# Kernel optimization log

Hardware: AMD Instinct MI355X
Metric: run time of the kernel (lower is better)

## Reference

```python
import math
import jax, jax.numpy as jnp
import numpy as np

CELL = 16
BLOCK = 2
NBINS = 9


def setup_inputs() -> dict:
    key = jax.random.key(0)
    im = jax.random.normal(key, (16, 3, 512, 512), dtype=jnp.float32)
    return {"im": im}


def _l2hys(x):
    # L2 normalize over (bh, bw, bins), clamp at 0.2, renormalize (L2-Hys)
    n1 = jnp.sqrt(jnp.sum(x * x, axis=(-1, -2, -3), keepdims=True))
    t = jnp.minimum(x / (n1 + 1e-10), 0.2)
    n2 = jnp.sqrt(jnp.sum(t * t, axis=(-1, -2, -3), keepdims=True))
    return t / (n2 + 1e-10)


def _hog_forward(im):
    B, C, H, W = im.shape
    cs, nb, bs = CELL, NBINS, BLOCK
    gain = nb / math.pi
    # complex Sobel kernel: real part = x-gradient, imag part = y-gradient
    kx = jnp.array([[-1., 0., 1.], [-2., 0., 2.], [-1., 0., 1.]], jnp.float32)
    ky = jnp.array([[-1., -2., -1.], [0., 0., 0.], [1., 2., 1.]], jnp.float32)
    imp = jnp.pad(im, ((0, 0), (0, 0), (1, 1), (1, 1)), mode="reflect")
    x = imp.reshape(B * C, 1, H + 2, W + 2)
    k = jnp.stack([kx, ky])[:, None]  # (2,1,3,3)
    g = jax.lax.conv_general_dilated(x, k, (1, 1), "VALID")  # (B*C,2,H,W) cross-correlation, matches F.conv2d
    gx = g[:, 0].reshape(B, C, H, W)
    gy = g[:, 1].reshape(B, C, H, W)
    Hc, Wc = H // cs, W // cs
    P = cs * cs

    def unfold_cells(a):  # (B,C,H,W) -> (B,C,Hc,Wc,cs*cs)
        return a.reshape(B, C, Hc, cs, Wc, cs).transpose(0, 1, 2, 4, 3, 5).reshape(B, C, Hc, Wc, P)

    gx = unfold_cells(gx)
    gy = unfold_cells(gy)
    norm = jnp.sqrt(gx * gx + gy * gy)  # complex magnitude
    # channelWise=False: pick the channel with max magnitude per pixel
    idx = jnp.argmax(norm, axis=1, keepdims=True)
    norm = jnp.take_along_axis(norm, idx, axis=1)
    gx = jnp.take_along_axis(gx, idx, axis=1)
    gy = jnp.take_along_axis(gy, idx, axis=1)
    phase = jnp.mod(jnp.arctan2(gy, gx), math.pi)  # complex angle mod pi

    # bilinear soft binning via scatter_add
    edges = jnp.linspace(0.0, math.pi, nb + 1)
    left = jnp.floor(gain * phase).astype(jnp.int32)
    prct = gain * (phase - edges[left])
    li = left % nb
    ri = (left + 1) % nb
    N = B * 1 * Hc * Wc
    rows = jnp.broadcast_to(jnp.arange(N)[:, None], (N, P))
    hist = jnp.zeros((N, nb), norm.dtype)
    hist = hist.at[rows, li.reshape(N, P)].add(((1.0 - prct) * norm).reshape(N, P))
    hist = hist.at[rows, ri.reshape(N, P)].add((prct * norm).reshape(N, P))
    hist = hist.reshape(B, 1, Hc, Wc, nb) / float(P)

    # block normalize: unfold cells into overlapping blocks (stride = blockSize//2)
    step = bs // 2
    Hb = (Hc - bs) // step + 1
    Wb = (Wc - bs) // step + 1
    blocks = jnp.stack(
        [
            jnp.stack(
                [hist[:, :, i:i + step * (Hb - 1) + 1:step, j:j + step * (Wb - 1) + 1:step, :] for j in range(bs)],
                axis=-2,
            )
            for i in range(bs)
        ],
        axis=-3,
    )  # (B,1,Hb,Wb,bs,bs,nb)
    return _l2hys(blocks)


def reference(im):
    return _hog_forward(im)
```

## Files before the change

kernel.cpp:

```cpp
#include <hip/hip_runtime.h>
#include <hip/hip_bf16.h>
#include <math.h>


#define IMG_H 512
#define IMG_W 512
#define NCH 3
#define NB_ 16
#define HC 32
#define WC 32
#define HB 31
#define WB 31
#define NBINS 9

__device__ __forceinline__ int refl(int i, int n) {
    if (i < 0) i = -i;
    else if (i >= n) i = 2 * n - 2 - i;
    return i;
}

__global__ __launch_bounds__(256) void hog_hist_kernel(const float* __restrict__ im,
                                                       float* __restrict__ hist) {
    const int bid = blockIdx.x;
    const int b   = bid >> 8;
    const int cy  = (bid >> 3) & 31;
    const int cxg = bid & 7;

    __shared__ __align__(16) float sT[NCH][18][72];
    __shared__ float swp[4][4][NBINS];

    const int t = threadIdx.x;

    const int y0 = cy * 16 - 1;
    const int x0 = cxg * 64;
    const float* imb = im + (size_t)b * NCH * IMG_H * IMG_W;

    {
        const int x4 = t & 15;
        const int r0 = t >> 4;
#pragma unroll
        for (int k = 0; k < 4; ++k) {
            int rowid = r0 + 16 * k;
            if (rowid < NCH * 18) {
                int c  = rowid / 18;
                int yy = rowid - c * 18;
                int gy = refl(y0 + yy, IMG_H);
                const float4 v = *(const float4*)(imb + ((size_t)c * IMG_H + gy) * IMG_W + x0 + 4 * x4);
                *(float4*)&sT[c][yy][4 + 4 * x4] = v;
            }
        }
        if (t < 108) {
            int side = t & 1;
            int rid  = t >> 1;
            int c    = rid / 18;
            int yy   = rid - c * 18;
            int gy   = refl(y0 + yy, IMG_H);
            int gx   = refl(side ? x0 + 64 : x0 - 1, IMG_W);
            sT[c][yy][side ? 68 : 3] = imb[((size_t)c * IMG_H + gy) * IMG_W + gx];
        }
    }
    __syncthreads();

    const int px = t & 63;
    const int pr = (t >> 6) * 4;
    const int lx = 4 + px;

    float bn[4]  = {-1.0f, -1.0f, -1.0f, -1.0f};
    float bgx[4] = {0, 0, 0, 0};
    float bgy[4] = {0, 0, 0, 0};

#pragma unroll
    for (int c = 0; c < NCH; ++c) {
        float a[6][3];
#pragma unroll
        for (int j = 0; j < 6; ++j) {
            a[j][0] = sT[c][pr + j][lx - 1];
            a[j][1] = sT[c][pr + j][lx];
            a[j][2] = sT[c][pr + j][lx + 1];
        }
#pragma unroll
        for (int p = 0; p < 4; ++p) {
            float gx = (a[p][2] - a[p][0]) + 2.0f * (a[p + 1][2] - a[p + 1][0]) + (a[p + 2][2] - a[p + 2][0]);
            float gy = (a[p + 2][0] - a[p][0]) + 2.0f * (a[p + 2][1] - a[p][1]) + (a[p + 2][2] - a[p][2]);
            float n = sqrtf(gx * gx + gy * gy);
            if (n > bn[p]) { bn[p] = n; bgx[p] = gx; bgy[p] = gy; }
        }
    }

    const float PI_F  = (float)M_PI;
    const float HPI_F = (float)(M_PI / 2.0);
    const float GAIN  = (float)(9.0 / M_PI);
    const float BINW  = (float)(M_PI / 9.0);
    const float C1  = 0.99997726f, C3 = -0.33262347f, C5 = 0.19354346f;
    const float C7  = -0.11643287f, C9 = 0.05265332f, C11 = -0.01172120f;

    float acc[NBINS];
#pragma unroll
    for (int k = 0; k < NBINS; ++k) acc[k] = 0.0f;

#pragma unroll
    for (int p = 0; p < 4; ++p) {
        float gx = bgx[p], gy = bgy[p], n = bn[p];
        float ax = fabsf(gx), ay = fabsf(gy);
        float mn = fminf(ax, ay), mx = fmaxf(ax, ay);
        float r  = __fdividef(mn, mx + 1e-37f);
        float r2 = r * r;
        float at = r * (C1 + r2 * (C3 + r2 * (C5 + r2 * (C7 + r2 * (C9 + r2 * C11)))));
        if (ay > ax) at = HPI_F - at;
        if ((__float_as_uint(gx) ^ __float_as_uint(gy)) & 0x80000000u) at = PI_F - at;

        float fp_ = GAIN * at;
        int left  = (int)floorf(fp_);
        float prct = GAIN * (at - (float)left * BINW);
        int li = (left >= NBINS) ? left - NBINS : left;
        int ri = (li == NBINS - 1) ? 0 : li + 1;

        float w_l = (1.0f - prct) * n;
        float w_r = prct * n;
#pragma unroll
        for (int k = 0; k < NBINS; ++k) {
            acc[k] += (li == k) ? w_l : 0.0f;
            acc[k] += (ri == k) ? w_r : 0.0f;
        }
    }

#pragma unroll
    for (int m = 1; m <= 8; m <<= 1) {
#pragma unroll
        for (int k = 0; k < NBINS; ++k)
            acc[k] += __shfl_xor(acc[k], m, 64);
    }

    const int lane = t & 63;
    const int wv   = t >> 6;
    if ((lane & 15) == 0) {
        const int cl = lane >> 4;
#pragma unroll
        for (int k = 0; k < NBINS; ++k) swp[wv][cl][k] = acc[k];
    }
    __syncthreads();

    if (t < 4 * NBINS) {
        int c_local = t / NBINS;
        int bin     = t - c_local * NBINS;
        float sum = swp[0][c_local][bin] + swp[1][c_local][bin]
                  + swp[2][c_local][bin] + swp[3][c_local][bin];
        int cellX   = cxg * 4 + c_local;
        size_t cell = ((size_t)b * HC + cy) * WC + cellX;
        hist[cell * NBINS + bin] = sum * (1.0f / 256.0f);
    }
}

__global__ __launch_bounds__(256) void hog_norm_kernel(const float* __restrict__ hist,
                                                       float* __restrict__ out) {
    int idx = blockIdx.x * 256 + threadIdx.x;
    if (idx >= NB_ * HB * WB) return;
    int b = idx / (HB * WB);
    int r = idx - b * (HB * WB);
    int i = r / WB;
    int j = r - i * WB;

    float v[36];
    float ss = 0.0f;
#pragma unroll
    for (int bi = 0; bi < 2; ++bi) {
#pragma unroll
        for (int bj = 0; bj < 2; ++bj) {
            const float* hp = hist + (size_t)(((b * HC) + (i + bi)) * WC + (j + bj)) * NBINS;
#pragma unroll
            for (int k = 0; k < NBINS; ++k) {
                float x = hp[k];
                v[(bi * 2 + bj) * NBINS + k] = x;
                ss += x * x;
            }
        }
    }
    float inv1 = 1.0f / (sqrtf(ss) + 1e-10f);
    float ss2 = 0.0f;
#pragma unroll
    for (int k = 0; k < 36; ++k) {
        float tt = fminf(v[k] * inv1, 0.2f);
        v[k] = tt;
        ss2 += tt * tt;
    }
    float inv2 = 1.0f / (sqrtf(ss2) + 1e-10f);
    float* op = out + (size_t)idx * 36;
#pragma unroll
    for (int k = 0; k < 36; ++k) op[k] = v[k] * inv2;
}

extern "C" void kernel_launch(void* const* d_in, const int* in_sizes, int n_in,
                              void* d_out, int out_size, void* d_ws, size_t ws_size,
                              hipStream_t stream) {
    const float* im = (const float*)d_in[0];
    float* out = (float*)d_out;
    float* hist = (float*)d_ws;

    hog_hist_kernel<<<NB_ * HC * 8, 256, 0, stream>>>(im, hist);

    int nout_blocks = NB_ * HB * WB;
    hog_norm_kernel<<<(nout_blocks + 255) / 256, 256, 0, stream>>>(hist, out);
}
```

Baseline: 36.89 us.

## Process two horizontal pixels per thread and use tent-function bin weights

Each block now covers a 128-pixel-wide strip (8 cells), and each thread computes two adjacent pixels, reusing the shared column differences across both Sobel stencils. The soft-binning switches from computing floor/left/right indices to a branchless tent weight fmax(1-|fp-k|,0) per bin, with bin 0 wrapping via fp-9. The shuffle reduction drops one level. This cuts redundant LDS reads and halo loads, but halves the grid size, which lowers parallelism.

```diff
diff --git a/kernel.cpp b/kernel.cpp
--- a/kernel.cpp
+++ b/kernel.cpp
@@ -22,25 +22,24 @@
 __global__ __launch_bounds__(256) void hog_hist_kernel(const float* __restrict__ im,
                                                        float* __restrict__ hist) {
     const int bid = blockIdx.x;
-    const int b   = bid >> 8;
-    const int cy  = (bid >> 3) & 31;
-    const int cxg = bid & 7;
-
-    __shared__ __align__(16) float sT[NCH][18][72];
-    __shared__ float swp[4][4][NBINS];
+    const int b   = bid >> 7;
+    const int cy  = (bid >> 2) & 31;
+    const int cxg = bid & 3;
+
+    __shared__ __align__(16) float sT[NCH][18][136];
+    __shared__ float swp[4][8][NBINS];
 
     const int t = threadIdx.x;
-
     const int y0 = cy * 16 - 1;
-    const int x0 = cxg * 64;
+    const int x0 = cxg * 128;
     const float* imb = im + (size_t)b * NCH * IMG_H * IMG_W;
 
     {
-        const int x4 = t & 15;
-        const int r0 = t >> 4;
-#pragma unroll
-        for (int k = 0; k < 4; ++k) {
-            int rowid = r0 + 16 * k;
+        const int x4 = t & 31;
+        const int rb = t >> 5;
+#pragma unroll
+        for (int k = 0; k < 7; ++k) {
+            int rowid = rb + 8 * k;
             if (rowid < NCH * 18) {
                 int c  = rowid / 18;
                 int yy = rowid - c * 18;
@@ -55,42 +54,59 @@
             int c    = rid / 18;
             int yy   = rid - c * 18;
             int gy   = refl(y0 + yy, IMG_H);
-            int gx   = refl(side ? x0 + 64 : x0 - 1, IMG_W);
-            sT[c][yy][side ? 68 : 3] = imb[((size_t)c * IMG_H + gy) * IMG_W + gx];
+            int gx   = refl(side ? x0 + 128 : x0 - 1, IMG_W);
+            sT[c][yy][side ? 132 : 3] = imb[((size_t)c * IMG_H + gy) * IMG_W + gx];
         }
     }
     __syncthreads();
 
-    const int px = t & 63;
-    const int pr = (t >> 6) * 4;
-    const int lx = 4 + px;
-
-    float bn[4]  = {-1.0f, -1.0f, -1.0f, -1.0f};
-    float bgx[4] = {0, 0, 0, 0};
-    float bgy[4] = {0, 0, 0, 0};
+    const int cp = t & 63;
+    const int rq = t >> 6;
+    const int pr = rq * 4;
+    const int lxm1 = 3 + 2 * cp;
+
+    float bn[2][4], bgx[2][4], bgy[2][4];
+#pragma unroll
+    for (int e = 0; e < 2; ++e)
+#pragma unroll
+        for (int p = 0; p < 4; ++p) { bn[e][p] = -1.0f; bgx[e][p] = 0.0f; bgy[e][p] = 0.0f; }
 
 #pragma unroll
     for (int c = 0; c < NCH; ++c) {
-        float a[6][3];
+        float a[6][4];
 #pragma unroll
         for (int j = 0; j < 6; ++j) {
-            a[j][0] = sT[c][pr + j][lx - 1];
-            a[j][1] = sT[c][pr + j][lx];
-            a[j][2] = sT[c][pr + j][lx + 1];
-        }
+            const float* rowp = &sT[c][pr + j][lxm1];
+            a[j][0] = rowp[0]; a[j][1] = rowp[1]; a[j][2] = rowp[2]; a[j][3] = rowp[3];
+        }
+        float rdE[6], rdO[6];
+#pragma unroll
+        for (int j = 0; j < 6; ++j) {
+            rdE[j] = a[j][2] - a[j][0];
+            rdO[j] = a[j][3] - a[j][1];
+        }
+        float cd[4][4];
+#pragma unroll
+        for (int p = 0; p < 4; ++p)
+#pragma unroll
+            for (int cc = 0; cc < 4; ++cc) cd[cc][p] = a[p + 2][cc] - a[p][cc];
+
 #pragma unroll
         for (int p = 0; p < 4; ++p) {
-            float gx = (a[p][2] - a[p][0]) + 2.0f * (a[p + 1][2] - a[p + 1][0]) + (a[p + 2][2] - a[p + 2][0]);
-            float gy = (a[p + 2][0] - a[p][0]) + 2.0f * (a[p + 2][1] - a[p][1]) + (a[p + 2][2] - a[p][2]);
-            float n = sqrtf(gx * gx + gy * gy);
-            if (n > bn[p]) { bn[p] = n; bgx[p] = gx; bgy[p] = gy; }
+            float gxE = (rdE[p] + 2.0f * rdE[p + 1]) + rdE[p + 2];
+            float gyE = (cd[0][p] + 2.0f * cd[1][p]) + cd[2][p];
+            float nE  = sqrtf(gxE * gxE + gyE * gyE);
+            if (nE > bn[0][p]) { bn[0][p] = nE; bgx[0][p] = gxE; bgy[0][p] = gyE; }
+            float gxO = (rdO[p] + 2.0f * rdO[p + 1]) + rdO[p + 2];
+            float gyO = (cd[1][p] + 2.0f * cd[2][p]) + cd[3][p];
+            float nO  = sqrtf(gxO * gxO + gyO * gyO);
+            if (nO > bn[1][p]) { bn[1][p] = nO; bgx[1][p] = gxO; bgy[1][p] = gyO; }
         }
     }
 
     const float PI_F  = (float)M_PI;
     const float HPI_F = (float)(M_PI / 2.0);
     const float GAIN  = (float)(9.0 / M_PI);
-    const float BINW  = (float)(M_PI / 9.0);
     const float C1  = 0.99997726f, C3 = -0.33262347f, C5 = 0.19354346f;
     const float C7  = -0.11643287f, C9 = 0.05265332f, C11 = -0.01172120f;
 
@@ -99,53 +115,49 @@
     for (int k = 0; k < NBINS; ++k) acc[k] = 0.0f;
 
 #pragma unroll
-    for (int p = 0; p < 4; ++p) {
-        float gx = bgx[p], gy = bgy[p], n = bn[p];
-        float ax = fabsf(gx), ay = fabsf(gy);
-        float mn = fminf(ax, ay), mx = fmaxf(ax, ay);
-        float r  = __fdividef(mn, mx + 1e-37f);
-        float r2 = r * r;
-        float at = r * (C1 + r2 * (C3 + r2 * (C5 + r2 * (C7 + r2 * (C9 + r2 * C11)))));
-        if (ay > ax) at = HPI_F - at;
-        if ((__float_as_uint(gx) ^ __float_as_uint(gy)) & 0x80000000u) at = PI_F - at;
-
-        float fp_ = GAIN * at;
-        int left  = (int)floorf(fp_);
-        float prct = GAIN * (at - (float)left * BINW);
-        int li = (left >= NBINS) ? left - NBINS : left;
-        int ri = (li == NBINS - 1) ? 0 : li + 1;
-
-        float w_l = (1.0f - prct) * n;
-        float w_r = prct * n;
-#pragma unroll
-        for (int k = 0; k < NBINS; ++k) {
-            acc[k] += (li == k) ? w_l : 0.0f;
-            acc[k] += (ri == k) ? w_r : 0.0f;
-        }
-    }
-
-#pragma unroll
-    for (int m = 1; m <= 8; m <<= 1) {
+    for (int e = 0; e < 2; ++e) {
+#pragma unroll
+        for (int p = 0; p < 4; ++p) {
+            float gx = bgx[e][p], gy = bgy[e][p], n = bn[e][p];
+            float ax = fabsf(gx), ay = fabsf(gy);
+            float mn = fminf(ax, ay), mx = fmaxf(ax, ay);
+            float r  = __fdividef(mn, mx + 1e-37f);
+            float r2 = r * r;
+            float at = r * (C1 + r2 * (C3 + r2 * (C5 + r2 * (C7 + r2 * (C9 + r2 * C11)))));
+            if (ay > ax) at = HPI_F - at;
+            if ((__float_as_uint(gx) ^ __float_as_uint(gy)) & 0x80000000u) at = PI_F - at;
+            float fp = GAIN * at;
+
+            float w0 = fmaxf(1.0f - fabsf(fp), 0.0f) + fmaxf(1.0f - fabsf(fp - 9.0f), 0.0f);
+            acc[0] = fmaf(w0, n, acc[0]);
+#pragma unroll
+            for (int k = 1; k < NBINS; ++k) {
+                float wk = fmaxf(1.0f - fabsf(fp - (float)k), 0.0f);
+                acc[k] = fmaf(wk, n, acc[k]);
+            }
+        }
+    }
+
+#pragma unroll
+    for (int m = 1; m <= 4; m <<= 1) {
 #pragma unroll
         for (int k = 0; k < NBINS; ++k)
             acc[k] += __shfl_xor(acc[k], m, 64);
     }
 
-    const int lane = t & 63;
-    const int wv   = t >> 6;
-    if ((lane & 15) == 0) {
-        const int cl = lane >> 4;
-#pragma unroll
-        for (int k = 0; k < NBINS; ++k) swp[wv][cl][k] = acc[k];
+    if ((cp & 7) == 0) {
+        const int cl = cp >> 3;
+#pragma unroll
+        for (int k = 0; k < NBINS; ++k) swp[rq][cl][k] = acc[k];
     }
     __syncthreads();
 
-    if (t < 4 * NBINS) {
-        int c_local = t / NBINS;
-        int bin     = t - c_local * NBINS;
-        float sum = swp[0][c_local][bin] + swp[1][c_local][bin]
-                  + swp[2][c_local][bin] + swp[3][c_local][bin];
-        int cellX   = cxg * 4 + c_local;
+    if (t < 8 * NBINS) {
+        int cl  = t / NBINS;
+        int bin = t - cl * NBINS;
+        float sum = swp[0][cl][bin] + swp[1][cl][bin]
+                  + swp[2][cl][bin] + swp[3][cl][bin];
+        int cellX = cxg * 8 + cl;
         size_t cell = ((size_t)b * HC + cy) * WC + cellX;
         hist[cell * NBINS + bin] = sum * (1.0f / 256.0f);
     }
@@ -196,7 +208,7 @@
     float* out = (float*)d_out;
     float* hist = (float*)d_ws;
 
-    hog_hist_kernel<<<NB_ * HC * 8, 256, 0, stream>>>(im, hist);
+    hog_hist_kernel<<<NB_ * HC * 4, 256, 0, stream>>>(im, hist);
 
     int nout_blocks = NB_ * HB * WB;
     hog_norm_kernel<<<(nout_blocks + 255) / 256, 256, 0, stream>>>(hist, out);
```

Result: faster. 35.22 us (-4.5%).
